# Kernel optimization log

Measured on AMD Instinct MI355X. Metric: run time of the kernel, lower is better.

Reference implementation:

```python
import jax, jax.numpy as jnp
import numpy as np

NB, NA, NC, NH, NW = 64, 5, 20, 38, 38
MAXT = 40
ANCHORS = jnp.array([[1.3221, 1.73145], [3.19275, 4.00944], [5.05587, 8.09892],
                     [9.47112, 4.84053], [11.2364, 10.0071]], dtype=jnp.float32)
OBJECT_SCALE, NOOBJECT_SCALE = 5.0, 1.0
CLASS_SCALE, COORD_SCALE = 1.0, 1.0
THRESH = 0.4


def setup_inputs() -> dict:
    key = jax.random.key(0)
    k1, k2, k3, k4 = jax.random.split(key, 4)
    output = jax.random.normal(k1, (NB, NA * (5 + NC), NH, NW), dtype=jnp.float32)
    cls_id = jax.random.randint(k2, (NB, MAXT), 0, NC).astype(jnp.float32)
    gxy = jax.random.uniform(k3, (NB, MAXT, 2), minval=0.05, maxval=0.95)
    gwh = jax.random.uniform(k4, (NB, MAXT, 2), minval=0.05, maxval=0.5)
    target = jnp.concatenate([cls_id[..., None], gxy, gwh], axis=-1).reshape(NB, MAXT * 5)
    return {"output": output, "target": target}


def iou_cwh(a, b):
    # boxes in (cx, cy, w, h)
    ax1, ax2 = a[..., 0] - a[..., 2] * 0.5, a[..., 0] + a[..., 2] * 0.5
    ay1, ay2 = a[..., 1] - a[..., 3] * 0.5, a[..., 1] + a[..., 3] * 0.5
    bx1, bx2 = b[..., 0] - b[..., 2] * 0.5, b[..., 0] + b[..., 2] * 0.5
    by1, by2 = b[..., 1] - b[..., 3] * 0.5, b[..., 1] + b[..., 3] * 0.5
    iw = jnp.maximum(jnp.minimum(ax2, bx2) - jnp.maximum(ax1, bx1), 0.0)
    ih = jnp.maximum(jnp.minimum(ay2, by2) - jnp.maximum(ay1, by1), 0.0)
    inter = iw * ih
    union = a[..., 2] * a[..., 3] + b[..., 2] * b[..., 3] - inter
    return inter / union


def smooth_l1_sum(p, t):
    d = jnp.abs(p - t)
    return jnp.sum(jnp.where(d < 1.0, 0.5 * d * d, d - 0.5))


def _forward(output, target):
    nB, nA, nC, nH, nW = NB, NA, NC, NH, NW
    out5 = output.reshape(nB, nA, 5 + nC, nH, nW)
    x = jax.nn.sigmoid(out5[:, :, 0])      # [nB,nA,nH,nW]
    y = jax.nn.sigmoid(out5[:, :, 1])
    w = out5[:, :, 2]
    h = out5[:, :, 3]
    conf = jax.nn.sigmoid(out5[:, :, 4])
    cls_logits = jnp.transpose(out5[:, :, 5:], (0, 1, 3, 4, 2))  # [nB,nA,nH,nW,nC]

    # --- decode predicted boxes (detached, mirrors use of .data in torch) ---
    sg = jax.lax.stop_gradient
    grid_x = jnp.arange(nW, dtype=jnp.float32)[None, None, None, :]
    grid_y = jnp.arange(nH, dtype=jnp.float32)[None, None, :, None]
    aw = ANCHORS[:, 0][None, :, None, None]
    ah = ANCHORS[:, 1][None, :, None, None]
    pred = jnp.stack([sg(x) + grid_x, sg(y) + grid_y,
                      jnp.exp(sg(w)) * aw, jnp.exp(sg(h)) * ah], axis=-1)  # [nB,nA,nH,nW,4]

    # --- build_targets (vectorized) ---
    tgt = target.reshape(nB, MAXT, 5)
    gcls = tgt[..., 0]
    gx, gy = tgt[..., 1] * nW, tgt[..., 2] * nH
    gw, gh = tgt[..., 3] * nW, tgt[..., 4] * nH
    # loop breaks at first zero gx: all later targets invalid
    valid = jnp.cumprod((tgt[..., 1] != 0).astype(jnp.float32), axis=1) > 0  # [nB,40]

    gt_boxes = jnp.stack([gx, gy, gw, gh], axis=-1)                 # [nB,40,4]
    pb = pred.reshape(nB, nA * nH * nW, 4)
    ious = iou_cwh(gt_boxes[:, :, None, :], pb[:, None, :, :])      # [nB,40,nAnchors]
    ious = jnp.where(valid[:, :, None], ious, 0.0)
    cur_ious = jnp.max(ious, axis=1)                                # [nB,nAnchors]
    conf_mask = jnp.where(cur_ious > THRESH, 0.0, NOOBJECT_SCALE).reshape(nB, nA, nH, nW)

    # best anchor per GT: IoU of zero-centered (w,h) boxes
    aws, ahs = ANCHORS[:, 0], ANCHORS[:, 1]
    inter = jnp.minimum(gw[..., None], aws) * jnp.minimum(gh[..., None], ahs)
    a_iou = inter / (gw[..., None] * gh[..., None] + aws * ahs - inter)  # [nB,40,nA]
    best_n = jnp.argmax(a_iou, axis=-1)                                  # [nB,40]

    gi = jnp.clip(gx.astype(jnp.int32), 0, nW - 1)
    gj = jnp.clip(gy.astype(jnp.int32), 0, nH - 1)
    bidx = jnp.broadcast_to(jnp.arange(nB)[:, None], (nB, MAXT))
    gi_s = jnp.where(valid, gi, nW)  # out-of-bounds -> dropped scatter
    idx = (bidx, best_n, gj, gi_s)

    pred_sel = pred[bidx, best_n, gj, gi]        # [nB,40,4]
    t_iou = iou_cwh(gt_boxes, pred_sel)          # [nB,40]
    aw_b, ah_b = aws[best_n], ahs[best_n]
    vtx = gx - gi.astype(jnp.float32)
    vty = gy - gj.astype(jnp.float32)
    vtw = jnp.log(gw / aw_b)
    vth = jnp.log(gh / ah_b)

    zeros = jnp.zeros((nB, nA, nH, nW), dtype=jnp.float32)
    coord_mask = zeros.at[idx].set(1.0, mode='drop')
    cls_mask = coord_mask  # identical writes in torch code
    conf_mask = conf_mask.at[idx].set(OBJECT_SCALE, mode='drop')
    tx = zeros.at[idx].set(vtx, mode='drop')
    ty = zeros.at[idx].set(vty, mode='drop')
    tw = zeros.at[idx].set(vtw, mode='drop')
    th = zeros.at[idx].set(vth, mode='drop')
    tconf = zeros.at[idx].set(t_iou, mode='drop')
    tcls = jnp.zeros((nB, nA, nH, nW), dtype=jnp.int32).at[idx].set(gcls.astype(jnp.int32), mode='drop')

    coord_mask = sg(coord_mask); cls_mask = sg(cls_mask)
    conf_mask = sg(conf_mask)
    tx, ty, tw, th, tconf = sg(tx), sg(ty), sg(tw), sg(th), sg(tconf)

    # --- losses ---
    loss_x = COORD_SCALE * smooth_l1_sum(x * coord_mask, tx * coord_mask) / 2.0
    loss_y = COORD_SCALE * smooth_l1_sum(y * coord_mask, ty * coord_mask) / 2.0
    loss_w = COORD_SCALE * smooth_l1_sum(w * coord_mask, tw * coord_mask) / 2.0
    loss_h = COORD_SCALE * smooth_l1_sum(h * coord_mask, th * coord_mask) / 2.0
    cm = jnp.sqrt(conf_mask)
    loss_conf = jnp.sum((conf * cm - tconf * cm) ** 2) / 2.0
    # focal loss (gamma=2, sum) over cls-masked locations
    logp = jax.nn.log_softmax(cls_logits, axis=-1)
    logpt = jnp.take_along_axis(logp, tcls[..., None], axis=-1)[..., 0]
    pt = jnp.exp(logpt)
    fl = -((1.0 - pt) ** 2) * logpt
    loss_cls = CLASS_SCALE * jnp.sum(cls_mask * fl)

    loss_box = loss_x + loss_y + loss_w + loss_h + loss_conf
    loss = loss_box + loss_cls
    return loss, loss_cls, loss_box


def reference(output, target):
    return _forward(output, target)
```

## Files before the change

### kernel.cpp

```cpp
#include <hip/hip_runtime.h>

#define NB 64
#define NA 5
#define NC 20
#define NH 38
#define NW 38
#define MAXT 40
#define CS (NH * NW)
#define CELLS_PER_B (NA * CS)
#define TPB 256
#define CPT 2
#define CHUNK_CELLS (TPB * CPT)
#define CHUNKS 15
#define NPART (NB * CHUNKS)

__constant__ float c_aw[NA] = {1.3221f, 3.19275f, 5.05587f, 9.47112f, 11.2364f};
__constant__ float c_ah[NA] = {1.73145f, 4.00944f, 8.09892f, 4.84053f, 10.0071f};

__device__ __forceinline__ float sl1(float d) {
    d = fabsf(d);
    return (d < 1.0f) ? 0.5f * d * d : d - 0.5f;
}
__device__ __forceinline__ float sigm(float x) {
    return __builtin_amdgcn_rcpf(1.0f + __expf(-x));
}

__global__ __launch_bounds__(TPB) void region_loss_kernel(
    const float* __restrict__ outp, const float* __restrict__ tgt,
    float2* __restrict__ partials)
{
    __shared__ float4 s_box[MAXT];
    __shared__ float  s_ga04[MAXT];
    __shared__ int    s_key[MAXT];

    const int b     = blockIdx.x / CHUNKS;
    const int chunk = blockIdx.x - b * CHUNKS;
    const int tid   = threadIdx.x;

    float w_gx = 0.f, w_gy = 0.f, w_gw = 0.f, w_gh = 0.f;
    int   w_bn = 0, w_gi = 0, w_gj = 0, w_cls = 0;
    bool  w_valid = false;

    if (tid < 64) {
        const bool is_t = tid < MAXT;
        const float* tb = tgt + b * (MAXT * 5) + tid * 5;
        float t0 = 0.f, t1 = 0.f, t2 = 0.f, t3 = 0.f, t4 = 0.f;
        if (is_t) { t0 = tb[0]; t1 = tb[1]; t2 = tb[2]; t3 = tb[3]; t4 = tb[4]; }
        const unsigned long long nz = __ballot(is_t && (t1 != 0.0f));
        const bool valid = is_t && ((~nz & (((1ull << tid) << 1) - 1ull)) == 0ull);
        if (is_t) {
            if (valid) {
                const float gx = t1 * NW, gy = t2 * NH, gw = t3 * NW, gh = t4 * NH;
                int bn = 0; float best = -1.0f;
                #pragma unroll
                for (int a = 0; a < NA; ++a) {
                    const float inter = fminf(gw, c_aw[a]) * fminf(gh, c_ah[a]);
                    const float aiou  = inter / (gw * gh + c_aw[a] * c_ah[a] - inter);
                    if (aiou > best) { best = aiou; bn = a; }
                }
                const int gi = min(max((int)gx, 0), NW - 1);
                const int gj = min(max((int)gy, 0), NH - 1);
                s_box[tid]  = make_float4(gx - 0.5f * gw, gy - 0.5f * gh,
                                          gx + 0.5f * gw, gy + 0.5f * gh);
                s_ga04[tid] = 0.4f * gw * gh;
                s_key[tid]  = bn * CS + gj * NW + gi;
                w_gx = gx; w_gy = gy; w_gw = gw; w_gh = gh;
                w_bn = bn; w_gi = gi; w_gj = gj; w_cls = (int)t0; w_valid = true;
            } else {
                s_box[tid]  = make_float4(3e30f, 3e30f, -3e30f, -3e30f);
                s_ga04[tid] = 0.0f;
                s_key[tid]  = -1;
            }
        }
    }
    __syncthreads();

    float box_sum = 0.0f, cls_sum = 0.0f;

    if (chunk == 0 && w_valid) {
        const int mykey = w_bn * CS + w_gj * NW + w_gi;
        bool last = true;
        for (int tp = tid + 1; tp < MAXT; ++tp) last &= (s_key[tp] != mykey);
        if (last) {
            const float* cell = outp + (size_t)((b * NA + w_bn) * (5 + NC)) * CS
                                + (w_gj * NW + w_gi);
            const float xo = cell[0],      yo = cell[CS];
            const float wo = cell[2 * CS], ho = cell[3 * CS], co = cell[4 * CS];
            float cls_v[NC];
            #pragma unroll
            for (int q = 0; q < NC; ++q) cls_v[q] = cell[(5 + q) * CS];

            const float sx = sigm(xo), sy = sigm(yo), sc = sigm(co);
            const float pxc = sx + (float)w_gi, pyc = sy + (float)w_gj;
            const float pw = __expf(wo) * c_aw[w_bn], ph = __expf(ho) * c_ah[w_bn];
            const float px1 = pxc - 0.5f * pw, px2 = pxc + 0.5f * pw;
            const float py1 = pyc - 0.5f * ph, py2 = pyc + 0.5f * ph;
            const float pa = pw * ph, p04 = 0.4f * pa;

            bool flag = false;
            for (int t = 0; t < MAXT; ++t) {
                const float4 bx = s_box[t];
                const float iw = fminf(px2, bx.z) - fmaxf(px1, bx.x);
                const float ih = fminf(py2, bx.w) - fmaxf(py1, bx.y);
                const float inter = fmaxf(iw, 0.0f) * fmaxf(ih, 0.0f);
                flag = flag | (1.4f * inter > p04 + s_ga04[t]);
            }
            const float cmd = flag ? 0.0f : 1.0f;

            const float gx1 = w_gx - 0.5f * w_gw, gx2 = w_gx + 0.5f * w_gw;
            const float gy1 = w_gy - 0.5f * w_gh, gy2 = w_gy + 0.5f * w_gh;
            const float iw = fminf(px2, gx2) - fmaxf(px1, gx1);
            const float ih = fminf(py2, gy2) - fmaxf(py1, gy1);
            const float inter = fmaxf(iw, 0.f) * fmaxf(ih, 0.f);
            const float tconf = inter / (w_gw * w_gh + pa - inter);

            const float dc = sc - tconf;
            box_sum += 2.5f * dc * dc - 0.5f * cmd * sc * sc;

            const float vtx = w_gx - (float)w_gi, vty = w_gy - (float)w_gj;
            const float vtw = __logf(w_gw / c_aw[w_bn]);
            const float vth = __logf(w_gh / c_ah[w_bn]);
            box_sum += 0.5f * (sl1(sx - vtx) + sl1(sy - vty) +
                               sl1(wo - vtw) + sl1(ho - vth));

            float m = -1e30f;
            #pragma unroll
            for (int q = 0; q < NC; ++q) m = fmaxf(m, cls_v[q]);
            float se = 0.f, lt = 0.f;
            #pragma unroll
            for (int q = 0; q < NC; ++q) {
                se += __expf(cls_v[q] - m);
                if (q == w_cls) lt = cls_v[q];
            }
            const float logpt = lt - (m + __logf(se));
            const float pt = __expf(logpt);
            const float om = 1.0f - pt;
            cls_sum += -(om * om) * logpt;
        }
    }

    const int cbase = chunk * CHUNK_CELLS + tid;
    float px1[CPT], px2[CPT], py1[CPT], py2[CPT], p04[CPT], scv[CPT];
    bool  flag[CPT];

    #pragma unroll
    for (int u = 0; u < CPT; ++u) {
        const int c = cbase + u * TPB;
        flag[u] = false;
        if (c < CELLS_PER_B) {
            const int a = c / CS, r = c - a * CS;
            const int j = r / NW,  i = r - j * NW;
            const float* cell = outp + (size_t)((b * NA + a) * (5 + NC)) * CS + r;
            const float xo = cell[0],      yo = cell[CS];
            const float wo = cell[2 * CS], ho = cell[3 * CS], co = cell[4 * CS];
            const float sx = sigm(xo), sy = sigm(yo);
            scv[u] = sigm(co);
            const float pxc = sx + (float)i, pyc = sy + (float)j;
            const float pw = __expf(wo) * c_aw[a], ph = __expf(ho) * c_ah[a];
            px1[u] = pxc - 0.5f * pw; px2[u] = pxc + 0.5f * pw;
            py1[u] = pyc - 0.5f * ph; py2[u] = pyc + 0.5f * ph;
            p04[u] = 0.4f * (pw * ph);
        } else {
            px1[u] = 3e30f; px2[u] = -3e30f;
            py1[u] = 3e30f; py2[u] = -3e30f;
            p04[u] = 0.0f;  scv[u] = 0.0f;
        }
    }

    #pragma unroll
    for (int t = 0; t < MAXT; ++t) {
        const float4 bx = s_box[t];
        const float  ga = s_ga04[t];
        #pragma unroll
        for (int u = 0; u < CPT; ++u) {
            const float iw = fminf(px2[u], bx.z) - fmaxf(px1[u], bx.x);
            const float ih = fminf(py2[u], bx.w) - fmaxf(py1[u], bx.y);
            const float inter = fmaxf(iw, 0.0f) * fmaxf(ih, 0.0f);
            flag[u] = flag[u] | (1.4f * inter > p04[u] + ga);
        }
    }

    #pragma unroll
    for (int u = 0; u < CPT; ++u) {
        const float cm = flag[u] ? 0.0f : 1.0f;
        box_sum += 0.5f * cm * scv[u] * scv[u];
    }

    #pragma unroll
    for (int off = 32; off > 0; off >>= 1) {
        box_sum += __shfl_down(box_sum, off);
        cls_sum += __shfl_down(cls_sum, off);
    }
    __shared__ float red[8];
    const int wv = tid >> 6, ln = tid & 63;
    if (ln == 0) { red[wv] = box_sum; red[4 + wv] = cls_sum; }
    __syncthreads();
    if (tid == 0) {
        partials[blockIdx.x] = make_float2(red[0] + red[1] + red[2] + red[3],
                                           red[4] + red[5] + red[6] + red[7]);
    }
}

__global__ __launch_bounds__(256) void finalize_kernel(
    const float2* __restrict__ partials, float* __restrict__ o)
{
    const int tid = threadIdx.x;
    float box = 0.0f, cls = 0.0f;
    for (int k = tid; k < NPART; k += 256) {
        const float2 p = partials[k];
        box += p.x; cls += p.y;
    }
    #pragma unroll
    for (int off = 32; off > 0; off >>= 1) {
        box += __shfl_down(box, off);
        cls += __shfl_down(cls, off);
    }
    __shared__ float red[8];
    const int wv = tid >> 6, ln = tid & 63;
    if (ln == 0) { red[wv] = box; red[4 + wv] = cls; }
    __syncthreads();
    if (tid == 0) {
        const float boxT = red[0] + red[1] + red[2] + red[3];
        const float clsT = red[4] + red[5] + red[6] + red[7];
        o[0] = boxT + clsT;
        o[1] = clsT;
        o[2] = boxT;
    }
}

extern "C" void kernel_launch(void* const* d_in, const int* in_sizes, int n_in,
                              void* d_out, int out_size, void* d_ws, size_t ws_size,
                              hipStream_t stream)
{
    const float* outp = (const float*)d_in[0];
    const float* tgt  = (const float*)d_in[1];
    float2* partials = (float2*)d_ws;

    region_loss_kernel<<<dim3(NPART), dim3(TPB), 0, stream>>>(outp, tgt, partials);
    finalize_kernel<<<1, 256, 0, stream>>>(partials, (float*)d_out);
}
```

Baseline: 19.93 us.

## Split target prep into separate kernel and use atomics instead of finalize pass

Target parsing, anchor matching and the per-target winner loss move into a small prep kernel that writes truth boxes to workspace. A dense kernel then handles 4 cells per thread over fewer chunks, reading the boxes from global memory. The blocks add their results straight into the output with atomics, which removes the finalize kernel. The aim is to stop every block redoing target setup and to stop chunk 0 serialising the winner work. In exchange the dense kernel must wait for the prep kernel, reads boxes from global instead of shared memory, and the atomic float adds make the summation order nondeterministic.

```diff
diff --git a/kernel.cpp b/kernel.cpp
--- a/kernel.cpp
+++ b/kernel.cpp
@@ -9,10 +9,9 @@
 #define CS (NH * NW)
 #define CELLS_PER_B (NA * CS)
 #define TPB 256
-#define CPT 2
+#define CPT 4
 #define CHUNK_CELLS (TPB * CPT)
-#define CHUNKS 15
-#define NPART (NB * CHUNKS)
+#define CHUNKS 8
 
 __constant__ float c_aw[NA] = {1.3221f, 3.19275f, 5.05587f, 9.47112f, 11.2364f};
 __constant__ float c_ah[NA] = {1.73145f, 4.00944f, 8.09892f, 4.84053f, 10.0071f};
@@ -25,60 +24,60 @@
     return __builtin_amdgcn_rcpf(1.0f + __expf(-x));
 }
 
-__global__ __launch_bounds__(TPB) void region_loss_kernel(
+__global__ __launch_bounds__(64) void prep_kernel(
     const float* __restrict__ outp, const float* __restrict__ tgt,
-    float2* __restrict__ partials)
+    float4* __restrict__ boxes,
+    float*  __restrict__ gas,
+    float2* __restrict__ winner,
+    float*  __restrict__ o)
 {
+    const int b   = blockIdx.x;
+    const int tid = threadIdx.x;
+    if (b == 0 && tid < 3) o[tid] = 0.0f;
+
     __shared__ float4 s_box[MAXT];
-    __shared__ float  s_ga04[MAXT];
+    __shared__ float  s_ga[MAXT];
     __shared__ int    s_key[MAXT];
 
-    const int b     = blockIdx.x / CHUNKS;
-    const int chunk = blockIdx.x - b * CHUNKS;
-    const int tid   = threadIdx.x;
+    const bool is_t = tid < MAXT;
+    const float* tb = tgt + b * (MAXT * 5) + tid * 5;
+    float t0 = 0.f, t1 = 0.f, t2 = 0.f, t3 = 0.f, t4 = 0.f;
+    if (is_t) { t0 = tb[0]; t1 = tb[1]; t2 = tb[2]; t3 = tb[3]; t4 = tb[4]; }
+    const unsigned long long nz = __ballot(is_t && (t1 != 0.0f));
+    const bool valid = is_t && ((~nz & (((1ull << tid) << 1) - 1ull)) == 0ull);
 
     float w_gx = 0.f, w_gy = 0.f, w_gw = 0.f, w_gh = 0.f;
-    int   w_bn = 0, w_gi = 0, w_gj = 0, w_cls = 0;
-    bool  w_valid = false;
-
-    if (tid < 64) {
-        const bool is_t = tid < MAXT;
-        const float* tb = tgt + b * (MAXT * 5) + tid * 5;
-        float t0 = 0.f, t1 = 0.f, t2 = 0.f, t3 = 0.f, t4 = 0.f;
-        if (is_t) { t0 = tb[0]; t1 = tb[1]; t2 = tb[2]; t3 = tb[3]; t4 = tb[4]; }
-        const unsigned long long nz = __ballot(is_t && (t1 != 0.0f));
-        const bool valid = is_t && ((~nz & (((1ull << tid) << 1) - 1ull)) == 0ull);
-        if (is_t) {
-            if (valid) {
-                const float gx = t1 * NW, gy = t2 * NH, gw = t3 * NW, gh = t4 * NH;
-                int bn = 0; float best = -1.0f;
-                #pragma unroll
-                for (int a = 0; a < NA; ++a) {
-                    const float inter = fminf(gw, c_aw[a]) * fminf(gh, c_ah[a]);
-                    const float aiou  = inter / (gw * gh + c_aw[a] * c_ah[a] - inter);
-                    if (aiou > best) { best = aiou; bn = a; }
-                }
-                const int gi = min(max((int)gx, 0), NW - 1);
-                const int gj = min(max((int)gy, 0), NH - 1);
-                s_box[tid]  = make_float4(gx - 0.5f * gw, gy - 0.5f * gh,
-                                          gx + 0.5f * gw, gy + 0.5f * gh);
-                s_ga04[tid] = 0.4f * gw * gh;
-                s_key[tid]  = bn * CS + gj * NW + gi;
-                w_gx = gx; w_gy = gy; w_gw = gw; w_gh = gh;
-                w_bn = bn; w_gi = gi; w_gj = gj; w_cls = (int)t0; w_valid = true;
-            } else {
-                s_box[tid]  = make_float4(3e30f, 3e30f, -3e30f, -3e30f);
-                s_ga04[tid] = 0.0f;
-                s_key[tid]  = -1;
+    int   w_bn = 0, w_gi = 0, w_gj = 0, w_cls = 0, mykey = -1;
+
+    if (is_t) {
+        float4 mybox = make_float4(3e30f, 3e30f, -3e30f, -3e30f);
+        float  myga  = 0.0f;
+        if (valid) {
+            const float gx = t1 * NW, gy = t2 * NH, gw = t3 * NW, gh = t4 * NH;
+            int bn = 0; float best = -1.0f;
+            #pragma unroll
+            for (int a = 0; a < NA; ++a) {
+                const float inter = fminf(gw, c_aw[a]) * fminf(gh, c_ah[a]);
+                const float aiou  = inter / (gw * gh + c_aw[a] * c_ah[a] - inter);
+                if (aiou > best) { best = aiou; bn = a; }
             }
-        }
+            const int gi = min(max((int)gx, 0), NW - 1);
+            const int gj = min(max((int)gy, 0), NH - 1);
+            mybox = make_float4(gx - 0.5f * gw, gy - 0.5f * gh,
+                                gx + 0.5f * gw, gy + 0.5f * gh);
+            myga  = 0.4f * gw * gh;
+            mykey = bn * CS + gj * NW + gi;
+            w_gx = gx; w_gy = gy; w_gw = gw; w_gh = gh;
+            w_bn = bn; w_gi = gi; w_gj = gj; w_cls = (int)t0;
+        }
+        s_box[tid] = mybox; s_ga[tid] = myga; s_key[tid] = valid ? mykey : -1;
+        boxes[b * MAXT + tid] = mybox;
+        gas[b * MAXT + tid]   = myga;
     }
     __syncthreads();
 
     float box_sum = 0.0f, cls_sum = 0.0f;
-
-    if (chunk == 0 && w_valid) {
-        const int mykey = w_bn * CS + w_gj * NW + w_gi;
+    if (valid) {
         bool last = true;
         for (int tp = tid + 1; tp < MAXT; ++tp) last &= (s_key[tp] != mykey);
         if (last) {
@@ -103,7 +102,7 @@
                 const float iw = fminf(px2, bx.z) - fmaxf(px1, bx.x);
                 const float ih = fminf(py2, bx.w) - fmaxf(py1, bx.y);
                 const float inter = fmaxf(iw, 0.0f) * fmaxf(ih, 0.0f);
-                flag = flag | (1.4f * inter > p04 + s_ga04[t]);
+                flag = flag | (1.4f * inter > p04 + s_ga[t]);
             }
             const float cmd = flag ? 0.0f : 1.0f;
 
@@ -138,6 +137,25 @@
             cls_sum += -(om * om) * logpt;
         }
     }
+
+    #pragma unroll
+    for (int off = 32; off > 0; off >>= 1) {
+        box_sum += __shfl_down(box_sum, off);
+        cls_sum += __shfl_down(cls_sum, off);
+    }
+    if (tid == 0) winner[b] = make_float2(box_sum, cls_sum);
+}
+
+__global__ __launch_bounds__(TPB) void dense_kernel(
+    const float* __restrict__ outp,
+    const float4* __restrict__ boxes, const float* __restrict__ gas,
+    const float2* __restrict__ winner, float* __restrict__ o)
+{
+    const int b     = blockIdx.x / CHUNKS;
+    const int chunk = blockIdx.x - b * CHUNKS;
+    const int tid   = threadIdx.x;
+    const float4* bb = boxes + b * MAXT;
+    const float*  gg = gas   + b * MAXT;
 
     const int cbase = chunk * CHUNK_CELLS + tid;
     float px1[CPT], px2[CPT], py1[CPT], py2[CPT], p04[CPT], scv[CPT];
@@ -167,10 +185,10 @@
         }
     }
 
-    #pragma unroll
+    #pragma unroll 8
     for (int t = 0; t < MAXT; ++t) {
-        const float4 bx = s_box[t];
-        const float  ga = s_ga04[t];
+        const float4 bx = bb[t];
+        const float  ga = gg[t];
         #pragma unroll
         for (int u = 0; u < CPT; ++u) {
             const float iw = fminf(px2[u], bx.z) - fmaxf(px1[u], bx.x);
@@ -180,6 +198,7 @@
         }
     }
 
+    float box_sum = 0.0f;
     #pragma unroll
     for (int u = 0; u < CPT; ++u) {
         const float cm = flag[u] ? 0.0f : 1.0f;
@@ -187,44 +206,21 @@
     }
 
     #pragma unroll
-    for (int off = 32; off > 0; off >>= 1) {
-        box_sum += __shfl_down(box_sum, off);
-        cls_sum += __shfl_down(cls_sum, off);
-    }
-    __shared__ float red[8];
+    for (int off = 32; off > 0; off >>= 1) box_sum += __shfl_down(box_sum, off);
+    __shared__ float red[4];
     const int wv = tid >> 6, ln = tid & 63;
-    if (ln == 0) { red[wv] = box_sum; red[4 + wv] = cls_sum; }
+    if (ln == 0) red[wv] = box_sum;
     __syncthreads();
     if (tid == 0) {
-        partials[blockIdx.x] = make_float2(red[0] + red[1] + red[2] + red[3],
-                                           red[4] + red[5] + red[6] + red[7]);
-    }
-}
-
-__global__ __launch_bounds__(256) void finalize_kernel(
-    const float2* __restrict__ partials, float* __restrict__ o)
-{
-    const int tid = threadIdx.x;
-    float box = 0.0f, cls = 0.0f;
-    for (int k = tid; k < NPART; k += 256) {
-        const float2 p = partials[k];
-        box += p.x; cls += p.y;
-    }
-    #pragma unroll
-    for (int off = 32; off > 0; off >>= 1) {
-        box += __shfl_down(box, off);
-        cls += __shfl_down(cls, off);
-    }
-    __shared__ float red[8];
-    const int wv = tid >> 6, ln = tid & 63;
-    if (ln == 0) { red[wv] = box; red[4 + wv] = cls; }
-    __syncthreads();
-    if (tid == 0) {
-        const float boxT = red[0] + red[1] + red[2] + red[3];
-        const float clsT = red[4] + red[5] + red[6] + red[7];
-        o[0] = boxT + clsT;
-        o[1] = clsT;
-        o[2] = boxT;
+        float box = red[0] + red[1] + red[2] + red[3];
+        float cls = 0.0f;
+        if (chunk == 0) {
+            const float2 wn = winner[b];
+            box += wn.x; cls = wn.y;
+            atomicAdd(&o[1], cls);
+        }
+        atomicAdd(&o[0], box + cls);
+        atomicAdd(&o[2], box);
     }
 }
 
@@ -234,8 +230,13 @@
 {
     const float* outp = (const float*)d_in[0];
     const float* tgt  = (const float*)d_in[1];
-    float2* partials = (float2*)d_ws;
-
-    region_loss_kernel<<<dim3(NPART), dim3(TPB), 0, stream>>>(outp, tgt, partials);
-    finalize_kernel<<<1, 256, 0, stream>>>(partials, (float*)d_out);
-}
+    float* o = (float*)d_out;
+
+    char* ws = (char*)d_ws;
+    float2* winner = (float2*)ws;
+    float4* boxes  = (float4*)(ws + 1024);
+    float*  gas    = (float*)(ws + 1024 + NB * MAXT * sizeof(float4));
+
+    prep_kernel<<<dim3(NB), dim3(64), 0, stream>>>(outp, tgt, boxes, gas, winner, o);
+    dense_kernel<<<dim3(NB * CHUNKS), dim3(TPB), 0, stream>>>(outp, boxes, gas, winner, o);
+}
```

Measured after the change: 31.28 us. 57.0% more time.

## Fuse finalize into main kernel via cooperative grid sync and fewer larger chunks

Applied to the files above, without the earlier changes.

Replaces the two-kernel design (per-block partials plus a single-block finalize launch) with one cooperative kernel that uses a grid-wide sync, after which block 0 reduces the 512 partials. Cells per thread go from 2 to 4 and chunks per batch from 15 to 8, shrinking the grid to 512 blocks so it can be co-resident. The per-target work moves to the last chunk, and the target loop is partially unrolled. This removes one kernel launch, at the cost of grid-sync overhead, cooperative-launch overhead, and fewer threads doing more serial work each.

```diff
diff --git a/kernel.cpp b/kernel.cpp
--- a/kernel.cpp
+++ b/kernel.cpp
@@ -1,4 +1,7 @@
 #include <hip/hip_runtime.h>
+#include <hip/hip_cooperative_groups.h>
+
+namespace cg = cooperative_groups;
 
 #define NB 64
 #define NA 5
@@ -9,10 +12,10 @@
 #define CS (NH * NW)
 #define CELLS_PER_B (NA * CS)
 #define TPB 256
-#define CPT 2
+#define CPT 4
 #define CHUNK_CELLS (TPB * CPT)
-#define CHUNKS 15
-#define NPART (NB * CHUNKS)
+#define CHUNKS 8
+#define NBLK (NB * CHUNKS)
 
 __constant__ float c_aw[NA] = {1.3221f, 3.19275f, 5.05587f, 9.47112f, 11.2364f};
 __constant__ float c_ah[NA] = {1.73145f, 4.00944f, 8.09892f, 4.84053f, 10.0071f};
@@ -25,12 +28,12 @@
     return __builtin_amdgcn_rcpf(1.0f + __expf(-x));
 }
 
-__global__ __launch_bounds__(TPB) void region_loss_kernel(
+__global__ __launch_bounds__(TPB) void region_one(
     const float* __restrict__ outp, const float* __restrict__ tgt,
-    float2* __restrict__ partials)
+    float2* __restrict__ partials, float* __restrict__ o)
 {
     __shared__ float4 s_box[MAXT];
-    __shared__ float  s_ga04[MAXT];
+    __shared__ float  s_ga[MAXT];
     __shared__ int    s_key[MAXT];
 
     const int b     = blockIdx.x / CHUNKS;
@@ -38,7 +41,7 @@
     const int tid   = threadIdx.x;
 
     float w_gx = 0.f, w_gy = 0.f, w_gw = 0.f, w_gh = 0.f;
-    int   w_bn = 0, w_gi = 0, w_gj = 0, w_cls = 0;
+    int   w_bn = 0, w_gi = 0, w_gj = 0, w_cls = 0, mykey = -1;
     bool  w_valid = false;
 
     if (tid < 64) {
@@ -49,6 +52,8 @@
         const unsigned long long nz = __ballot(is_t && (t1 != 0.0f));
         const bool valid = is_t && ((~nz & (((1ull << tid) << 1) - 1ull)) == 0ull);
         if (is_t) {
+            float4 mybox = make_float4(3e30f, 3e30f, -3e30f, -3e30f);
+            float  myga  = 0.0f;
             if (valid) {
                 const float gx = t1 * NW, gy = t2 * NH, gw = t3 * NW, gh = t4 * NH;
                 int bn = 0; float best = -1.0f;
@@ -60,25 +65,21 @@
                 }
                 const int gi = min(max((int)gx, 0), NW - 1);
                 const int gj = min(max((int)gy, 0), NH - 1);
-                s_box[tid]  = make_float4(gx - 0.5f * gw, gy - 0.5f * gh,
-                                          gx + 0.5f * gw, gy + 0.5f * gh);
-                s_ga04[tid] = 0.4f * gw * gh;
-                s_key[tid]  = bn * CS + gj * NW + gi;
+                mybox = make_float4(gx - 0.5f * gw, gy - 0.5f * gh,
+                                    gx + 0.5f * gw, gy + 0.5f * gh);
+                myga  = 0.4f * gw * gh;
+                mykey = bn * CS + gj * NW + gi;
                 w_gx = gx; w_gy = gy; w_gw = gw; w_gh = gh;
                 w_bn = bn; w_gi = gi; w_gj = gj; w_cls = (int)t0; w_valid = true;
-            } else {
-                s_box[tid]  = make_float4(3e30f, 3e30f, -3e30f, -3e30f);
-                s_ga04[tid] = 0.0f;
-                s_key[tid]  = -1;
-            }
+            }
+            s_box[tid] = mybox; s_ga[tid] = myga; s_key[tid] = valid ? mykey : -1;
         }
     }
     __syncthreads();
 
     float box_sum = 0.0f, cls_sum = 0.0f;
 
-    if (chunk == 0 && w_valid) {
-        const int mykey = w_bn * CS + w_gj * NW + w_gi;
+    if (chunk == CHUNKS - 1 && w_valid) {
         bool last = true;
         for (int tp = tid + 1; tp < MAXT; ++tp) last &= (s_key[tp] != mykey);
         if (last) {
@@ -103,7 +104,7 @@
                 const float iw = fminf(px2, bx.z) - fmaxf(px1, bx.x);
                 const float ih = fminf(py2, bx.w) - fmaxf(py1, bx.y);
                 const float inter = fmaxf(iw, 0.0f) * fmaxf(ih, 0.0f);
-                flag = flag | (1.4f * inter > p04 + s_ga04[t]);
+                flag = flag | (1.4f * inter > p04 + s_ga[t]);
             }
             const float cmd = flag ? 0.0f : 1.0f;
 
@@ -139,51 +140,53 @@
         }
     }
 
-    const int cbase = chunk * CHUNK_CELLS + tid;
-    float px1[CPT], px2[CPT], py1[CPT], py2[CPT], p04[CPT], scv[CPT];
-    bool  flag[CPT];
-
-    #pragma unroll
-    for (int u = 0; u < CPT; ++u) {
-        const int c = cbase + u * TPB;
-        flag[u] = false;
-        if (c < CELLS_PER_B) {
-            const int a = c / CS, r = c - a * CS;
-            const int j = r / NW,  i = r - j * NW;
-            const float* cell = outp + (size_t)((b * NA + a) * (5 + NC)) * CS + r;
-            const float xo = cell[0],      yo = cell[CS];
-            const float wo = cell[2 * CS], ho = cell[3 * CS], co = cell[4 * CS];
-            const float sx = sigm(xo), sy = sigm(yo);
-            scv[u] = sigm(co);
-            const float pxc = sx + (float)i, pyc = sy + (float)j;
-            const float pw = __expf(wo) * c_aw[a], ph = __expf(ho) * c_ah[a];
-            px1[u] = pxc - 0.5f * pw; px2[u] = pxc + 0.5f * pw;
-            py1[u] = pyc - 0.5f * ph; py2[u] = pyc + 0.5f * ph;
-            p04[u] = 0.4f * (pw * ph);
-        } else {
-            px1[u] = 3e30f; px2[u] = -3e30f;
-            py1[u] = 3e30f; py2[u] = -3e30f;
-            p04[u] = 0.0f;  scv[u] = 0.0f;
-        }
-    }
-
-    #pragma unroll
-    for (int t = 0; t < MAXT; ++t) {
-        const float4 bx = s_box[t];
-        const float  ga = s_ga04[t];
+    {
+        const int cbase = chunk * CHUNK_CELLS + tid;
+        float px1[CPT], px2[CPT], py1[CPT], py2[CPT], p04[CPT], scv[CPT];
+        bool  flag[CPT];
+
         #pragma unroll
         for (int u = 0; u < CPT; ++u) {
-            const float iw = fminf(px2[u], bx.z) - fmaxf(px1[u], bx.x);
-            const float ih = fminf(py2[u], bx.w) - fmaxf(py1[u], bx.y);
-            const float inter = fmaxf(iw, 0.0f) * fmaxf(ih, 0.0f);
-            flag[u] = flag[u] | (1.4f * inter > p04[u] + ga);
-        }
-    }
-
-    #pragma unroll
-    for (int u = 0; u < CPT; ++u) {
-        const float cm = flag[u] ? 0.0f : 1.0f;
-        box_sum += 0.5f * cm * scv[u] * scv[u];
+            const int c = cbase + u * TPB;
+            flag[u] = false;
+            if (c < CELLS_PER_B) {
+                const int a = c / CS, r = c - a * CS;
+                const int j = r / NW,  i = r - j * NW;
+                const float* cell = outp + (size_t)((b * NA + a) * (5 + NC)) * CS + r;
+                const float xo = cell[0],      yo = cell[CS];
+                const float wo = cell[2 * CS], ho = cell[3 * CS], co = cell[4 * CS];
+                const float sx = sigm(xo), sy = sigm(yo);
+                scv[u] = sigm(co);
+                const float pxc = sx + (float)i, pyc = sy + (float)j;
+                const float pw = __expf(wo) * c_aw[a], ph = __expf(ho) * c_ah[a];
+                px1[u] = pxc - 0.5f * pw; px2[u] = pxc + 0.5f * pw;
+                py1[u] = pyc - 0.5f * ph; py2[u] = pyc + 0.5f * ph;
+                p04[u] = 0.4f * (pw * ph);
+            } else {
+                px1[u] = 3e30f; px2[u] = -3e30f;
+                py1[u] = 3e30f; py2[u] = -3e30f;
+                p04[u] = 0.0f;  scv[u] = 0.0f;
+            }
+        }
+
+        #pragma unroll 8
+        for (int t = 0; t < MAXT; ++t) {
+            const float4 bx = s_box[t];
+            const float  ga = s_ga[t];
+            #pragma unroll
+            for (int u = 0; u < CPT; ++u) {
+                const float iw = fminf(px2[u], bx.z) - fmaxf(px1[u], bx.x);
+                const float ih = fminf(py2[u], bx.w) - fmaxf(py1[u], bx.y);
+                const float inter = fmaxf(iw, 0.0f) * fmaxf(ih, 0.0f);
+                flag[u] = flag[u] | (1.4f * inter > p04[u] + ga);
+            }
+        }
+
+        #pragma unroll
+        for (int u = 0; u < CPT; ++u) {
+            const float cm = flag[u] ? 0.0f : 1.0f;
+            box_sum += 0.5f * cm * scv[u] * scv[u];
+        }
     }
 
     #pragma unroll
@@ -198,33 +201,30 @@
     if (tid == 0) {
         partials[blockIdx.x] = make_float2(red[0] + red[1] + red[2] + red[3],
                                            red[4] + red[5] + red[6] + red[7]);
-    }
-}
-
-__global__ __launch_bounds__(256) void finalize_kernel(
-    const float2* __restrict__ partials, float* __restrict__ o)
-{
-    const int tid = threadIdx.x;
-    float box = 0.0f, cls = 0.0f;
-    for (int k = tid; k < NPART; k += 256) {
-        const float2 p = partials[k];
-        box += p.x; cls += p.y;
-    }
-    #pragma unroll
-    for (int off = 32; off > 0; off >>= 1) {
-        box += __shfl_down(box, off);
-        cls += __shfl_down(cls, off);
-    }
-    __shared__ float red[8];
-    const int wv = tid >> 6, ln = tid & 63;
-    if (ln == 0) { red[wv] = box; red[4 + wv] = cls; }
-    __syncthreads();
-    if (tid == 0) {
-        const float boxT = red[0] + red[1] + red[2] + red[3];
-        const float clsT = red[4] + red[5] + red[6] + red[7];
-        o[0] = boxT + clsT;
-        o[1] = clsT;
-        o[2] = boxT;
+        __threadfence();
+    }
+
+    cg::this_grid().sync();
+
+    if (blockIdx.x == 0) {
+        const float2 pa = partials[tid];
+        const float2 pb = partials[tid + 256];
+        float box = pa.x + pb.x;
+        float cls = pa.y + pb.y;
+        #pragma unroll
+        for (int off = 32; off > 0; off >>= 1) {
+            box += __shfl_down(box, off);
+            cls += __shfl_down(cls, off);
+        }
+        if (ln == 0) { red[wv] = box; red[4 + wv] = cls; }
+        __syncthreads();
+        if (tid == 0) {
+            const float boxT = red[0] + red[1] + red[2] + red[3];
+            const float clsT = red[4] + red[5] + red[6] + red[7];
+            o[0] = boxT + clsT;
+            o[1] = clsT;
+            o[2] = boxT;
+        }
     }
 }
 
@@ -234,8 +234,10 @@
 {
     const float* outp = (const float*)d_in[0];
     const float* tgt  = (const float*)d_in[1];
-    float2* partials = (float2*)d_ws;
-
-    region_loss_kernel<<<dim3(NPART), dim3(TPB), 0, stream>>>(outp, tgt, partials);
-    finalize_kernel<<<1, 256, 0, stream>>>(partials, (float*)d_out);
-}
+    float2* partials  = (float2*)d_ws;
+    float*  o         = (float*)d_out;
+
+    void* args[] = { (void*)&outp, (void*)&tgt, (void*)&partials, (void*)&o };
+    hipLaunchCooperativeKernel((const void*)region_one, dim3(NBLK), dim3(TPB),
+                               args, 0, stream);
+}
```

Result: slower. 75.25 us (+277.6%).
